# Kernel optimization log

Hardware: AMD Instinct MI355X
Metric: run time of the kernel (lower is better)

The kernel has to match this reference:

```python
import jax, jax.numpy as jnp
import numpy as np

N = 10000   # num_nodes
E = 320000  # num_edges
D = 256     # feature / hidden dim
H = 256


def adj_lap(edge_index, n):
    """Dense normalized adjacency (gcn_norm, no self loops) and sym Laplacian."""
    row, col = edge_index[0], edge_index[1]
    # dense 0/1 adjacency (duplicate edges overwrite with same value, as in the loop)
    A = jnp.zeros((n, n), dtype=jnp.float32).at[row, col].set(1.0)
    # gcn_norm: deg = scatter(w, col) -> column sums
    deg_c = A.sum(axis=0)
    dinv_c = jnp.where(deg_c > 0, jax.lax.rsqrt(jnp.maximum(deg_c, 1e-12)), 0.0)
    anorm = dinv_c[:, None] * A * dinv_c[None, :]
    # get_laplacian 'sym': deg = scatter(w, row) -> row sums; L = I - D^-1/2 A D^-1/2
    deg_r = A.sum(axis=1)
    dinv_r = jnp.where(deg_r > 0, jax.lax.rsqrt(jnp.maximum(deg_r, 1e-12)), 0.0)
    lap = jnp.eye(n, dtype=jnp.float32) - dinv_r[:, None] * A * dinv_r[None, :]
    return lap, anorm


def gcn2(x, M, W1, b1, W2, b2):
    # pretrain_model: two-layer spectral GCN using propagation matrix M
    h = jax.nn.relu(M @ (x @ W1) + b1)
    return M @ (h @ W2) + b2


def setup_inputs() -> dict:
    key = jax.random.key(0)
    k1, k2, k3, k4 = jax.random.split(key, 4)
    x = jax.random.normal(k1, (N, D), dtype=jnp.float32)
    edge_index = jax.random.randint(k2, (2, E), 0, N, dtype=jnp.int64)
    W1 = jax.random.normal(k3, (D, H), dtype=jnp.float32) * 0.05
    b1 = jnp.zeros((H,), dtype=jnp.float32)
    W2 = jax.random.normal(k4, (H, H), dtype=jnp.float32) * 0.05
    b2 = jnp.zeros((H,), dtype=jnp.float32)
    return {"x": x, "edge_index": edge_index, "W1": W1, "b1": b1, "W2": W2, "b2": b2}


def reference(x, edge_index, W1, b1, W2, b2):
    # identity augmentor: x1 = x2 = x, edge_index1 = edge_index2 = edge_index,
    # so adj_lap is identical for both branches (computed once).
    lsym, anorm = adj_lap(edge_index, x.shape[0])
    z1 = gcn2(x, lsym, W1, b1, W2, b2)   # 'high' pass
    z2 = gcn2(x, anorm, W1, b1, W2, b2)  # 'low' pass
    z = z2
    return (z, z1, z2)
```

## Files before the change

kernel.cpp:

```cpp
#include <hip/hip_runtime.h>

#define NN 10000
#define EE 320000
#define HH 256
#define BKT 192

typedef __attribute__((ext_vector_type(8))) short bf16x8;
typedef __attribute__((ext_vector_type(4))) float f32x4;

__device__ float bf2f(unsigned int v) {
    return __uint_as_float(v << 16);
}
__device__ unsigned short f2bf(float f) {
    unsigned int i = __float_as_uint(f);
    return (unsigned short)((i + 0x7fffu + ((i >> 16) & 1u)) >> 16);
}
__device__ unsigned int fp8e(float f) {
    float a = fabsf(f);
    a = fminf(a, 448.0f);
    unsigned int bits = __float_as_uint(a * __uint_as_float(0x03800000u));
    bits = bits + 0x7ffffu + ((bits >> 20) & 1u);
    unsigned int r = bits >> 20;
    if (r > 0x7eu) r = 0x7eu;
    return r | ((__float_as_uint(f) >> 24) & 0x80u);
}
__device__ float fp8d(unsigned int b) {
    float mag = __uint_as_float((b & 0x7fu) << 20) * __uint_as_float(0x7B800000u);
    return __uint_as_float(((b & 0x80u) << 24) | __float_as_uint(mag));
}
__device__ unsigned int pk2(unsigned short a, unsigned short b) {
    return (unsigned int)a | ((unsigned int)b << 16);
}
__device__ int eload(const void* ei, int is64, int idx) {
    if (is64) return (int)(((const long long*)ei)[idx]);
    return ((const int*)ei)[idx];
}
__device__ __forceinline__ float dinv_of(int d) {
    return d > 0 ? rsqrtf((float)d) : 0.0f;
}

__global__ void k_A(const void* x, const void* ei, const void* W1, const void* W2,
                    int* flags, int* rawcnt, unsigned short* W1sw,
                    unsigned short* W2sw) {
    int b = blockIdx.x, t = threadIdx.x;
    if (b >= 65) {
        int idx = (b - 65) * 256 + t;
        ((uint4*)rawcnt)[idx] = make_uint4(0, 0, 0, 0);
        return;
    }
    if (b == 0) {
        __shared__ int s0, s1;
        if (t == 0) { s0 = 0; s1 = 0; }
        __syncthreads();
        if (t < 64) {
            const unsigned int* eu = (const unsigned int*)ei;
            const unsigned int* xu = (const unsigned int*)x;
            for (int k = t; k < 256; k += 64)
                if (eu[2 * k + 1] != 0) atomicOr(&s0, 1);
            unsigned int lo = xu[t] & 0xffffu;
            unsigned int ex = (lo >> 7) & 0xffu;
            if (lo == 0u || (ex >= 90u && ex <= 150u)) atomicAdd(&s1, 1);
        }
        __syncthreads();
        if (t == 0) {
            flags[0] = s0 ? 0 : 1;
            flags[1] = (s1 >= 56) ? 0 : 1;
        }
        return;
    }
    __shared__ int plaus;
    if (t == 0) plaus = 0;
    __syncthreads();
    if (t < 64) {
        unsigned int lo = ((const unsigned int*)x)[t] & 0xffffu;
        unsigned int ex = (lo >> 7) & 0xffu;
        if (lo == 0u || (ex >= 90u && ex <= 150u)) atomicAdd(&plaus, 1);
    }
    __syncthreads();
    int f32io = (plaus >= 56) ? 0 : 1;
    int vb = b - 1;
    const void* W = (vb < 32) ? W1 : W2;
    unsigned short* O = (vb < 32) ? W1sw : W2sw;
    int g = ((vb < 32) ? vb : vb - 32) * 256 + t;
    int gl = g & 63;
    int n = (g >> 6) & 15;
    int ks = g >> 10;
    int coln = n * 16 + (gl & 15);
    int krow = ks * 32 + ((gl >> 4) & 3) * 8;
    unsigned short v[8];
    if (f32io) {
        const float* Wf = (const float*)W;
        #pragma unroll
        for (int j = 0; j < 8; j++) v[j] = f2bf(Wf[(size_t)(krow + j) * HH + coln]);
    } else {
        const unsigned short* Wh = (const unsigned short*)W;
        #pragma unroll
        for (int j = 0; j < 8; j++) v[j] = Wh[(size_t)(krow + j) * HH + coln];
    }
    uint4 p;
    p.x = pk2(v[0], v[1]); p.y = pk2(v[2], v[3]);
    p.z = pk2(v[4], v[5]); p.w = pk2(v[6], v[7]);
    *(uint4*)(O + (size_t)g * 8) = p;
}

__global__ void k_B(const void* x, const void* ei, const unsigned short* W1sw,
                    const int* flags, int* rawcnt, unsigned short* bucket,
                    unsigned char* Yf8, void* Oout) {
    int b = blockIdx.x;
    int tid = threadIdx.x;
    if (b >= 625) {
        int e = (b - 625) * 256 + tid;
        if (e >= EE) return;
        int is64 = flags[0];
        int r = eload(ei, is64, e);
        int c = eload(ei, is64, EE + e);
        if (r < 0 || r >= NN || c < 0 || c >= NN) return;
        int slot = atomicAdd(&rawcnt[r], 1);
        if (slot < BKT) bucket[(size_t)r * BKT + slot] = (unsigned short)c;
        return;
    }
    __shared__ unsigned short As[16][264];
    int r0 = b * 16;
    int af32 = flags[1];
    {
        int row = tid >> 4, seg = tid & 15;
        if (af32) {
            const float* ap = (const float*)x + (size_t)(r0 + row) * HH + seg * 16;
            unsigned short v[16];
            #pragma unroll
            for (int j = 0; j < 16; j += 4) {
                float4 q = *(const float4*)(ap + j);
                v[j] = f2bf(q.x); v[j + 1] = f2bf(q.y);
                v[j + 2] = f2bf(q.z); v[j + 3] = f2bf(q.w);
            }
            uint4 p0, p1;
            p0.x = pk2(v[0], v[1]);   p0.y = pk2(v[2], v[3]);
            p0.z = pk2(v[4], v[5]);   p0.w = pk2(v[6], v[7]);
            p1.x = pk2(v[8], v[9]);   p1.y = pk2(v[10], v[11]);
            p1.z = pk2(v[12], v[13]); p1.w = pk2(v[14], v[15]);
            *(uint4*)&As[row][seg * 16] = p0;
            *(uint4*)&As[row][seg * 16 + 8] = p1;
        } else {
            const unsigned short* ap = (const unsigned short*)x + (size_t)(r0 + row) * HH + seg * 16;
            *(uint4*)&As[row][seg * 16] = *(const uint4*)ap;
            *(uint4*)&As[row][seg * 16 + 8] = *(const uint4*)(ap + 8);
        }
    }
    __syncthreads();
    int wv = tid >> 6;
    int lane = tid & 63;
    int quad = lane >> 4;
    int l16 = lane & 15;
    f32x4 acc[4] = {{0,0,0,0},{0,0,0,0},{0,0,0,0},{0,0,0,0}};
    for (int ks = 0; ks < 8; ks++) {
        bf16x8 af = *(const bf16x8*)&As[l16][ks * 32 + quad * 8];
        #pragma unroll
        for (int t = 0; t < 4; t++) {
            int n = wv * 4 + t;
            bf16x8 bf = *(const bf16x8*)(W1sw + ((size_t)(ks * 16 + n) * 64 + lane) * 8);
            acc[t] = __builtin_amdgcn_mfma_f32_16x16x32_bf16(af, bf, acc[t], 0, 0, 0);
        }
    }
    size_t chunkW = (size_t)NN * HH;
    #pragma unroll
    for (int t = 0; t < 4; t++) {
        int cn = (wv * 4 + t) * 16 + l16;
        #pragma unroll
        for (int r = 0; r < 4; r++) {
            int row = r0 + quad * 4 + r;
            float vv = acc[t][r];
            size_t idx = (size_t)row * HH + cn;
            Yf8[idx] = (unsigned char)fp8e(vv);
            if (af32) ((float*)Oout)[2 * chunkW + idx] = vv;
            else      ((unsigned short*)Oout)[2 * chunkW + idx] = f2bf(vv);
        }
    }
}

__global__ void k_DD(const int* rawcnt, int* cnt2, unsigned short* bucket) {
    __shared__ unsigned int bm[4][316];
    __shared__ int cnt[4];
    int wave = threadIdx.x >> 6;
    int lane = threadIdx.x & 63;
    int i = blockIdx.x * 4 + wave;
    int d = rawcnt[i];
    if (d > BKT) d = BKT;
    for (int t = lane; t < 313; t += 64) bm[wave][t] = 0u;
    if (lane == 0) cnt[wave] = 0;
    unsigned short* bp = bucket + (size_t)i * BKT;
    int cvals[3];
    int nt = 0;
    for (int t = lane; t < d; t += 64) cvals[nt++] = (int)bp[t];
    for (int k = 0; k < nt; k++) {
        int c = cvals[k];
        unsigned int m = 1u << (c & 31);
        unsigned int old = atomicOr(&bm[wave][c >> 5], m);
        if (!(old & m)) {
            int p = atomicAdd(&cnt[wave], 1);
            bp[p] = (unsigned short)c;
            atomicAdd(&cnt2[2 * c + 1], 1);
        }
    }
    if (lane == 0) atomicExch(&cnt2[2 * i], cnt[wave]);
}

__global__ void k_C(const unsigned char* Yf8, const void* Oout,
                    const unsigned short* bucket, const int* cnt2,
                    const void* bias, const int* flags,
                    unsigned short* H1, unsigned short* H2) {
    int wave = threadIdx.x >> 6;
    int lane = threadIdx.x & 63;
    int fb = lane * 4;
    int i = blockIdx.x * 4 + wave;
    float a1[4] = {0, 0, 0, 0};
    float a2[4] = {0, 0, 0, 0};
    int2 ddi = *(const int2*)(cnt2 + 2 * i);
    int n = ddi.x;
    const unsigned short* cp = bucket + (size_t)i * BKT;
    int t = 0;
    for (; t + 4 <= n; t += 4) {
        ushort4 c4 = *(const ushort4*)(cp + t);
        int cx[4] = {(int)c4.x, (int)c4.y, (int)c4.z, (int)c4.w};
        float wx[4], wy[4];
        #pragma unroll
        for (int j = 0; j < 4; j++) {
            int2 dd = *(const int2*)(cnt2 + 2 * cx[j]);
            wx[j] = dinv_of(dd.x);
            wy[j] = dinv_of(dd.y);
        }
        unsigned int gv[4];
        #pragma unroll
        for (int j = 0; j < 4; j++)
            gv[j] = *(const unsigned int*)(Yf8 + (size_t)cx[j] * 256 + fb);
        #pragma unroll
        for (int j = 0; j < 4; j++) {
            #pragma unroll
            for (int k = 0; k < 4; k++) {
                float y = fp8d((gv[j] >> (8 * k)) & 0xffu);
                a1[k] += wx[j] * y;
                a2[k] += wy[j] * y;
            }
        }
    }
    for (; t < n; t++) {
        int c = (int)cp[t];
        int2 dd = *(const int2*)(cnt2 + 2 * c);
        float wx = dinv_of(dd.x);
        float wy = dinv_of(dd.y);
        unsigned int g = *(const unsigned int*)(Yf8 + (size_t)c * 256 + fb);
        #pragma unroll
        for (int k = 0; k < 4; k++) {
            float y = fp8d((g >> (8 * k)) & 0xffu);
            a1[k] += wx * y;
            a2[k] += wy * y;
        }
    }
    int f32io = flags[1];
    float bv[4];
    if (f32io) {
        const float* bp = (const float*)bias + fb;
        #pragma unroll
        for (int k = 0; k < 4; k++) bv[k] = bp[k];
    } else {
        uint2 br = *(const uint2*)((const unsigned short*)bias + fb);
        bv[0] = bf2f(br.x & 0xffffu); bv[1] = bf2f(br.x >> 16);
        bv[2] = bf2f(br.y & 0xffffu); bv[3] = bf2f(br.y >> 16);
    }
    float wiix = dinv_of(ddi.x);
    float wiiy = dinv_of(ddi.y);
    size_t chunkW = (size_t)NN * HH;
    float yv[4];
    if (f32io) {
        const float* sp = (const float*)Oout + 2 * chunkW + (size_t)i * HH + fb;
        #pragma unroll
        for (int k = 0; k < 4; k++) yv[k] = sp[k];
    } else {
        uint2 yi = *(const uint2*)((const unsigned short*)Oout + 2 * chunkW + (size_t)i * HH + fb);
        yv[0] = bf2f(yi.x & 0xffffu); yv[1] = bf2f(yi.x >> 16);
        yv[2] = bf2f(yi.y & 0xffffu); yv[3] = bf2f(yi.y >> 16);
    }
    float h1[4], h2[4];
    #pragma unroll
    for (int k = 0; k < 4; k++) {
        h1[k] = fmaxf(0.f, yv[k] - wiix * a1[k] + bv[k]);
        h2[k] = fmaxf(0.f, wiiy * a2[k] + bv[k]);
    }
    uint2 p1, p2;
    p1.x = pk2(f2bf(h1[0]), f2bf(h1[1])); p1.y = pk2(f2bf(h1[2]), f2bf(h1[3]));
    p2.x = pk2(f2bf(h2[0]), f2bf(h2[1])); p2.y = pk2(f2bf(h2[2]), f2bf(h2[3]));
    *(uint2*)(H1 + (size_t)i * HH + fb) = p1;
    *(uint2*)(H2 + (size_t)i * HH + fb) = p2;
}

__global__ void k_D(const unsigned short* H1, const unsigned short* H2,
                    const unsigned short* Bsw, unsigned char* G12f8,
                    void* Oout, const int* flags) {
    __shared__ unsigned short As[16][264];
    int b = blockIdx.x;
    int tid = threadIdx.x;
    int isG1 = (b < 625);
    const unsigned short* A = isG1 ? H1 : H2;
    int r0 = (isG1 ? b : b - 625) * 16;
    {
        int row = tid >> 4, seg = tid & 15;
        const unsigned short* ap = A + (size_t)(r0 + row) * HH + seg * 16;
        *(uint4*)&As[row][seg * 16] = *(const uint4*)ap;
        *(uint4*)&As[row][seg * 16 + 8] = *(const uint4*)(ap + 8);
    }
    __syncthreads();
    int wv = tid >> 6;
    int lane = tid & 63;
    int quad = lane >> 4;
    int l16 = lane & 15;
    f32x4 acc[4] = {{0,0,0,0},{0,0,0,0},{0,0,0,0},{0,0,0,0}};
    for (int ks = 0; ks < 8; ks++) {
        bf16x8 af = *(const bf16x8*)&As[l16][ks * 32 + quad * 8];
        #pragma unroll
        for (int t = 0; t < 4; t++) {
            int n = wv * 4 + t;
            bf16x8 bf = *(const bf16x8*)(Bsw + ((size_t)(ks * 16 + n) * 64 + lane) * 8);
            acc[t] = __builtin_amdgcn_mfma_f32_16x16x32_bf16(af, bf, acc[t], 0, 0, 0);
        }
    }
    size_t chunkW = (size_t)NN * HH;
    int f32io = flags[1];
    #pragma unroll
    for (int t = 0; t < 4; t++) {
        int cn = (wv * 4 + t) * 16 + l16;
        #pragma unroll
        for (int r = 0; r < 4; r++) {
            int row = r0 + quad * 4 + r;
            float vv = acc[t][r];
            if (isG1) {
                G12f8[(size_t)row * 512 + cn] = (unsigned char)fp8e(vv);
                size_t idx = (size_t)row * HH + cn;
                if (f32io) ((float*)Oout)[chunkW + idx] = vv;
                else       ((unsigned short*)Oout)[chunkW + idx] = f2bf(vv);
            } else {
                G12f8[(size_t)row * 512 + 256 + cn] = (unsigned char)fp8e(vv);
            }
        }
    }
}

__global__ void k_E(const unsigned char* G12f8, const unsigned short* bucket,
                    const int* cnt2, const void* bias, const int* flags,
                    void* Oout) {
    int wave = threadIdx.x >> 6;
    int lane = threadIdx.x & 63;
    int half = lane >> 5;
    int sub = lane & 31;
    int fb = sub * 8;
    int goff = half * 256 + fb;
    int i = blockIdx.x * 4 + wave;
    float acc[8] = {0, 0, 0, 0, 0, 0, 0, 0};
    int2 ddi = *(const int2*)(cnt2 + 2 * i);
    int n = ddi.x;
    const unsigned short* cp = bucket + (size_t)i * BKT;
    int t = 0;
    for (; t + 4 <= n; t += 4) {
        ushort4 c4 = *(const ushort4*)(cp + t);
        int cx[4] = {(int)c4.x, (int)c4.y, (int)c4.z, (int)c4.w};
        float ws[4];
        #pragma unroll
        for (int j = 0; j < 4; j++) {
            int2 dd = *(const int2*)(cnt2 + 2 * cx[j]);
            ws[j] = dinv_of(half ? dd.y : dd.x);
        }
        uint2 gv[4];
        #pragma unroll
        for (int j = 0; j < 4; j++)
            gv[j] = *(const uint2*)(G12f8 + (size_t)cx[j] * 512 + goff);
        #pragma unroll
        for (int j = 0; j < 4; j++) {
            #pragma unroll
            for (int k = 0; k < 4; k++) {
                float y = fp8d((gv[j].x >> (8 * k)) & 0xffu);
                acc[k] += ws[j] * y;
            }
            #pragma unroll
            for (int k = 0; k < 4; k++) {
                float y = fp8d((gv[j].y >> (8 * k)) & 0xffu);
                acc[4 + k] += ws[j] * y;
            }
        }
    }
    for (; t < n; t++) {
        int c = (int)cp[t];
        int2 dd = *(const int2*)(cnt2 + 2 * c);
        float wsel = dinv_of(half ? dd.y : dd.x);
        uint2 g = *(const uint2*)(G12f8 + (size_t)c * 512 + goff);
        #pragma unroll
        for (int k = 0; k < 4; k++) acc[k] += wsel * fp8d((g.x >> (8 * k)) & 0xffu);
        #pragma unroll
        for (int k = 0; k < 4; k++) acc[4 + k] += wsel * fp8d((g.y >> (8 * k)) & 0xffu);
    }
    int f32io = flags[1];
    float bv[8];
    if (f32io) {
        const float* bp = (const float*)bias + fb;
        #pragma unroll
        for (int k = 0; k < 8; k++) bv[k] = bp[k];
    } else {
        uint4 br = *(const uint4*)((const unsigned short*)bias + fb);
        bv[0] = bf2f(br.x & 0xffffu); bv[1] = bf2f(br.x >> 16);
        bv[2] = bf2f(br.y & 0xffffu); bv[3] = bf2f(br.y >> 16);
        bv[4] = bf2f(br.z & 0xffffu); bv[5] = bf2f(br.z >> 16);
        bv[6] = bf2f(br.w & 0xffffu); bv[7] = bf2f(br.w >> 16);
    }
    size_t base = (size_t)i * HH + fb;
    size_t chunkW = (size_t)NN * HH;
    float z[8];
    if (half == 0) {
        float wiix = dinv_of(ddi.x);
        float gvv[8];
        if (f32io) {
            const float* sp = (const float*)Oout + chunkW + base;
            #pragma unroll
            for (int k = 0; k < 8; k++) gvv[k] = sp[k];
        } else {
            uint4 gi = *(const uint4*)((const unsigned short*)Oout + chunkW + base);
            gvv[0] = bf2f(gi.x & 0xffffu); gvv[1] = bf2f(gi.x >> 16);
            gvv[2] = bf2f(gi.y & 0xffffu); gvv[3] = bf2f(gi.y >> 16);
            gvv[4] = bf2f(gi.z & 0xffffu); gvv[5] = bf2f(gi.z >> 16);
            gvv[6] = bf2f(gi.w & 0xffffu); gvv[7] = bf2f(gi.w >> 16);
        }
        #pragma unroll
        for (int k = 0; k < 8; k++) z[k] = gvv[k] - wiix * acc[k] + bv[k];
        if (f32io) {
            float* o = (float*)Oout + chunkW + base;
            *(float4*)o = make_float4(z[0], z[1], z[2], z[3]);
            *(float4*)(o + 4) = make_float4(z[4], z[5], z[6], z[7]);
        } else {
            uint4 p;
            p.x = pk2(f2bf(z[0]), f2bf(z[1])); p.y = pk2(f2bf(z[2]), f2bf(z[3]));
            p.z = pk2(f2bf(z[4]), f2bf(z[5])); p.w = pk2(f2bf(z[6]), f2bf(z[7]));
            *(uint4*)((unsigned short*)Oout + chunkW + base) = p;
        }
    } else {
        float wiiy = dinv_of(ddi.y);
        #pragma unroll
        for (int k = 0; k < 8; k++) z[k] = wiiy * acc[k] + bv[k];
        if (f32io) {
            float* o0 = (float*)Oout + base;
            float* o2 = (float*)Oout + 2 * chunkW + base;
            float4 pa = make_float4(z[0], z[1], z[2], z[3]);
            float4 pb = make_float4(z[4], z[5], z[6], z[7]);
            *(float4*)o0 = pa; *(float4*)(o0 + 4) = pb;
            *(float4*)o2 = pa; *(float4*)(o2 + 4) = pb;
        } else {
            uint4 p;
            p.x = pk2(f2bf(z[0]), f2bf(z[1])); p.y = pk2(f2bf(z[2]), f2bf(z[3]));
            p.z = pk2(f2bf(z[4]), f2bf(z[5])); p.w = pk2(f2bf(z[6]), f2bf(z[7]));
            *(uint4*)((unsigned short*)Oout + base) = p;
            *(uint4*)((unsigned short*)Oout + 2 * chunkW + base) = p;
        }
    }
}

extern "C" void kernel_launch(void* const* d_in, const int* in_sizes, int n_in,
                              void* d_out, int out_size, void* d_ws, size_t ws_size,
                              hipStream_t stream) {
    const void* x = 0; const void* ei = 0;
    const void* W1 = 0; const void* b1 = 0; const void* W2 = 0; const void* b2 = 0;
    for (int i = 0; i < n_in; i++) {
        int s = in_sizes[i];
        if (s == NN * HH) x = d_in[i];
        else if (s == 2 * EE) ei = d_in[i];
        else if (s == HH * HH) { if (!W1) W1 = d_in[i]; else W2 = d_in[i]; }
        else if (s == HH) { if (!b1) b1 = d_in[i]; else b2 = d_in[i]; }
    }

    char* ws = (char*)d_ws;
    size_t off = 0;
    int* flags = (int*)(ws + off); off += 256;
    int* rawcnt = (int*)(ws + off); off += 40960;
    int* cnt2 = (int*)(ws + off); off += 81920;
    unsigned short* bucket = (unsigned short*)(ws + off); off += (size_t)NN * BKT * 2;
    unsigned short* W1sw = (unsigned short*)(ws + off); off += (size_t)HH * HH * 2;
    unsigned short* W2sw = (unsigned short*)(ws + off); off += (size_t)HH * HH * 2;
    unsigned char* Yf8 = (unsigned char*)(ws + off); off += (size_t)NN * 256;
    unsigned char* G12f8 = (unsigned char*)(ws + off); off += (size_t)NN * 512;
    unsigned short* H1 = (unsigned short*)(ws + off); off += (size_t)NN * HH * 2;
    unsigned short* H2 = (unsigned short*)(ws + off); off += (size_t)NN * HH * 2;

    k_A<<<95, 256, 0, stream>>>(x, ei, W1, W2, flags, rawcnt, W1sw, W2sw);
    k_B<<<1875, 256, 0, stream>>>(x, ei, W1sw, flags, rawcnt, bucket, Yf8, d_out);
    k_DD<<<NN / 4, 256, 0, stream>>>(rawcnt, cnt2, bucket);
    k_C<<<NN / 4, 256, 0, stream>>>(Yf8, d_out, bucket, cnt2, b1, flags, H1, H2);
    k_D<<<1250, 256, 0, stream>>>(H1, H2, W2sw, G12f8, d_out, flags);
    k_E<<<NN / 4, 256, 0, stream>>>(G12f8, bucket, cnt2, b2, flags, d_out);
}
```

Measured before the change: 204.4 us.

## Fuse sparse aggregation and W2 GEMM into one kernel via shared-memory H tiles

Merges the first-layer sparse aggregation (k_C) and the second dense GEMM (k_D) into a single kernel. Each 512-thread block aggregates 16 rows, keeps the bf16 H1/H2 tiles in LDS, then runs MFMA against W2 directly. This removes the global H1/H2 round trip and one launch. The cost is only 625 blocks of 512 threads, which lowers parallelism for the gather phase on a large GPU.

```diff
diff --git a/kernel.cpp b/kernel.cpp
--- a/kernel.cpp
+++ b/kernel.cpp
@@ -204,141 +204,128 @@
     if (lane == 0) atomicExch(&cnt2[2 * i], cnt[wave]);
 }
 
-__global__ void k_C(const unsigned char* Yf8, const void* Oout,
-                    const unsigned short* bucket, const int* cnt2,
-                    const void* bias, const int* flags,
-                    unsigned short* H1, unsigned short* H2) {
-    int wave = threadIdx.x >> 6;
-    int lane = threadIdx.x & 63;
+__global__ __launch_bounds__(512) void k_CD(
+        const unsigned char* Yf8, const unsigned short* bucket,
+        const int* cnt2, const unsigned short* W2sw, const void* b1,
+        const int* flags, unsigned char* G12f8, void* Oout) {
+    __shared__ unsigned short H1s[16][264];
+    __shared__ unsigned short H2s[16][264];
+    int tid = threadIdx.x;
+    int wave = tid >> 6;
+    int lane = tid & 63;
     int fb = lane * 4;
-    int i = blockIdx.x * 4 + wave;
-    float a1[4] = {0, 0, 0, 0};
-    float a2[4] = {0, 0, 0, 0};
-    int2 ddi = *(const int2*)(cnt2 + 2 * i);
-    int n = ddi.x;
-    const unsigned short* cp = bucket + (size_t)i * BKT;
-    int t = 0;
-    for (; t + 4 <= n; t += 4) {
-        ushort4 c4 = *(const ushort4*)(cp + t);
-        int cx[4] = {(int)c4.x, (int)c4.y, (int)c4.z, (int)c4.w};
-        float wx[4], wy[4];
-        #pragma unroll
-        for (int j = 0; j < 4; j++) {
-            int2 dd = *(const int2*)(cnt2 + 2 * cx[j]);
-            wx[j] = dinv_of(dd.x);
-            wy[j] = dinv_of(dd.y);
-        }
-        unsigned int gv[4];
-        #pragma unroll
-        for (int j = 0; j < 4; j++)
-            gv[j] = *(const unsigned int*)(Yf8 + (size_t)cx[j] * 256 + fb);
-        #pragma unroll
-        for (int j = 0; j < 4; j++) {
-            #pragma unroll
-            for (int k = 0; k < 4; k++) {
-                float y = fp8d((gv[j] >> (8 * k)) & 0xffu);
-                a1[k] += wx[j] * y;
-                a2[k] += wy[j] * y;
-            }
-        }
-    }
-    for (; t < n; t++) {
-        int c = (int)cp[t];
-        int2 dd = *(const int2*)(cnt2 + 2 * c);
-        float wx = dinv_of(dd.x);
-        float wy = dinv_of(dd.y);
-        unsigned int g = *(const unsigned int*)(Yf8 + (size_t)c * 256 + fb);
-        #pragma unroll
-        for (int k = 0; k < 4; k++) {
-            float y = fp8d((g >> (8 * k)) & 0xffu);
-            a1[k] += wx * y;
-            a2[k] += wy * y;
-        }
-    }
+    int bbase = blockIdx.x * 16;
     int f32io = flags[1];
+    size_t chunkW = (size_t)NN * HH;
     float bv[4];
     if (f32io) {
-        const float* bp = (const float*)bias + fb;
+        const float* bp = (const float*)b1 + fb;
         #pragma unroll
         for (int k = 0; k < 4; k++) bv[k] = bp[k];
     } else {
-        uint2 br = *(const uint2*)((const unsigned short*)bias + fb);
+        uint2 br = *(const uint2*)((const unsigned short*)b1 + fb);
         bv[0] = bf2f(br.x & 0xffffu); bv[1] = bf2f(br.x >> 16);
         bv[2] = bf2f(br.y & 0xffffu); bv[3] = bf2f(br.y >> 16);
     }
-    float wiix = dinv_of(ddi.x);
-    float wiiy = dinv_of(ddi.y);
-    size_t chunkW = (size_t)NN * HH;
-    float yv[4];
-    if (f32io) {
-        const float* sp = (const float*)Oout + 2 * chunkW + (size_t)i * HH + fb;
-        #pragma unroll
-        for (int k = 0; k < 4; k++) yv[k] = sp[k];
-    } else {
-        uint2 yi = *(const uint2*)((const unsigned short*)Oout + 2 * chunkW + (size_t)i * HH + fb);
-        yv[0] = bf2f(yi.x & 0xffffu); yv[1] = bf2f(yi.x >> 16);
-        yv[2] = bf2f(yi.y & 0xffffu); yv[3] = bf2f(yi.y >> 16);
-    }
-    float h1[4], h2[4];
-    #pragma unroll
-    for (int k = 0; k < 4; k++) {
-        h1[k] = fmaxf(0.f, yv[k] - wiix * a1[k] + bv[k]);
-        h2[k] = fmaxf(0.f, wiiy * a2[k] + bv[k]);
-    }
-    uint2 p1, p2;
-    p1.x = pk2(f2bf(h1[0]), f2bf(h1[1])); p1.y = pk2(f2bf(h1[2]), f2bf(h1[3]));
-    p2.x = pk2(f2bf(h2[0]), f2bf(h2[1])); p2.y = pk2(f2bf(h2[2]), f2bf(h2[3]));
-    *(uint2*)(H1 + (size_t)i * HH + fb) = p1;
-    *(uint2*)(H2 + (size_t)i * HH + fb) = p2;
-}
-
-__global__ void k_D(const unsigned short* H1, const unsigned short* H2,
-                    const unsigned short* Bsw, unsigned char* G12f8,
-                    void* Oout, const int* flags) {
-    __shared__ unsigned short As[16][264];
-    int b = blockIdx.x;
-    int tid = threadIdx.x;
-    int isG1 = (b < 625);
-    const unsigned short* A = isG1 ? H1 : H2;
-    int r0 = (isG1 ? b : b - 625) * 16;
-    {
-        int row = tid >> 4, seg = tid & 15;
-        const unsigned short* ap = A + (size_t)(r0 + row) * HH + seg * 16;
-        *(uint4*)&As[row][seg * 16] = *(const uint4*)ap;
-        *(uint4*)&As[row][seg * 16 + 8] = *(const uint4*)(ap + 8);
+    for (int rr = 0; rr < 2; rr++) {
+        int lr = wave * 2 + rr;
+        int i = bbase + lr;
+        float a1[4] = {0, 0, 0, 0};
+        float a2[4] = {0, 0, 0, 0};
+        int2 ddi = *(const int2*)(cnt2 + 2 * i);
+        int n = ddi.x;
+        const unsigned short* cp = bucket + (size_t)i * BKT;
+        int t = 0;
+        for (; t + 4 <= n; t += 4) {
+            ushort4 c4 = *(const ushort4*)(cp + t);
+            int cx[4] = {(int)c4.x, (int)c4.y, (int)c4.z, (int)c4.w};
+            float wx[4], wy[4];
+            #pragma unroll
+            for (int j = 0; j < 4; j++) {
+                int2 dd = *(const int2*)(cnt2 + 2 * cx[j]);
+                wx[j] = dinv_of(dd.x);
+                wy[j] = dinv_of(dd.y);
+            }
+            unsigned int gv[4];
+            #pragma unroll
+            for (int j = 0; j < 4; j++)
+                gv[j] = *(const unsigned int*)(Yf8 + (size_t)cx[j] * 256 + fb);
+            #pragma unroll
+            for (int j = 0; j < 4; j++) {
+                #pragma unroll
+                for (int k = 0; k < 4; k++) {
+                    float y = fp8d((gv[j] >> (8 * k)) & 0xffu);
+                    a1[k] += wx[j] * y;
+                    a2[k] += wy[j] * y;
+                }
+            }
+        }
+        for (; t < n; t++) {
+            int c = (int)cp[t];
+            int2 dd = *(const int2*)(cnt2 + 2 * c);
+            float wx = dinv_of(dd.x);
+            float wy = dinv_of(dd.y);
+            unsigned int g = *(const unsigned int*)(Yf8 + (size_t)c * 256 + fb);
+            #pragma unroll
+            for (int k = 0; k < 4; k++) {
+                float y = fp8d((g >> (8 * k)) & 0xffu);
+                a1[k] += wx * y;
+                a2[k] += wy * y;
+            }
+        }
+        float wiix = dinv_of(ddi.x);
+        float wiiy = dinv_of(ddi.y);
+        float yv[4];
+        if (f32io) {
+            const float* sp = (const float*)Oout + 2 * chunkW + (size_t)i * HH + fb;
+            #pragma unroll
+            for (int k = 0; k < 4; k++) yv[k] = sp[k];
+        } else {
+            uint2 yi = *(const uint2*)((const unsigned short*)Oout + 2 * chunkW + (size_t)i * HH + fb);
+            yv[0] = bf2f(yi.x & 0xffffu); yv[1] = bf2f(yi.x >> 16);
+            yv[2] = bf2f(yi.y & 0xffffu); yv[3] = bf2f(yi.y >> 16);
+        }
+        float h1[4], h2[4];
+        #pragma unroll
+        for (int k = 0; k < 4; k++) {
+            h1[k] = fmaxf(0.f, yv[k] - wiix * a1[k] + bv[k]);
+            h2[k] = fmaxf(0.f, wiiy * a2[k] + bv[k]);
+        }
+        uint2 p1, p2;
+        p1.x = pk2(f2bf(h1[0]), f2bf(h1[1])); p1.y = pk2(f2bf(h1[2]), f2bf(h1[3]));
+        p2.x = pk2(f2bf(h2[0]), f2bf(h2[1])); p2.y = pk2(f2bf(h2[2]), f2bf(h2[3]));
+        *(uint2*)&H1s[lr][fb] = p1;
+        *(uint2*)&H2s[lr][fb] = p2;
     }
     __syncthreads();
-    int wv = tid >> 6;
-    int lane = tid & 63;
     int quad = lane >> 4;
     int l16 = lane & 15;
-    f32x4 acc[4] = {{0,0,0,0},{0,0,0,0},{0,0,0,0},{0,0,0,0}};
+    f32x4 acc1[2] = {{0,0,0,0},{0,0,0,0}};
+    f32x4 acc2[2] = {{0,0,0,0},{0,0,0,0}};
     for (int ks = 0; ks < 8; ks++) {
-        bf16x8 af = *(const bf16x8*)&As[l16][ks * 32 + quad * 8];
-        #pragma unroll
-        for (int t = 0; t < 4; t++) {
-            int n = wv * 4 + t;
-            bf16x8 bf = *(const bf16x8*)(Bsw + ((size_t)(ks * 16 + n) * 64 + lane) * 8);
-            acc[t] = __builtin_amdgcn_mfma_f32_16x16x32_bf16(af, bf, acc[t], 0, 0, 0);
-        }
-    }
-    size_t chunkW = (size_t)NN * HH;
-    int f32io = flags[1];
+        bf16x8 af1 = *(const bf16x8*)&H1s[l16][ks * 32 + quad * 8];
+        bf16x8 af2 = *(const bf16x8*)&H2s[l16][ks * 32 + quad * 8];
+        #pragma unroll
+        for (int t = 0; t < 2; t++) {
+            int n = wave * 2 + t;
+            bf16x8 bf = *(const bf16x8*)(W2sw + ((size_t)(ks * 16 + n) * 64 + lane) * 8);
+            acc1[t] = __builtin_amdgcn_mfma_f32_16x16x32_bf16(af1, bf, acc1[t], 0, 0, 0);
+            acc2[t] = __builtin_amdgcn_mfma_f32_16x16x32_bf16(af2, bf, acc2[t], 0, 0, 0);
+        }
+    }
     #pragma unroll
-    for (int t = 0; t < 4; t++) {
-        int cn = (wv * 4 + t) * 16 + l16;
+    for (int t = 0; t < 2; t++) {
+        int cn = (wave * 2 + t) * 16 + l16;
         #pragma unroll
         for (int r = 0; r < 4; r++) {
-            int row = r0 + quad * 4 + r;
-            float vv = acc[t][r];
-            if (isG1) {
-                G12f8[(size_t)row * 512 + cn] = (unsigned char)fp8e(vv);
-                size_t idx = (size_t)row * HH + cn;
-                if (f32io) ((float*)Oout)[chunkW + idx] = vv;
-                else       ((unsigned short*)Oout)[chunkW + idx] = f2bf(vv);
-            } else {
-                G12f8[(size_t)row * 512 + 256 + cn] = (unsigned char)fp8e(vv);
-            }
+            int row = bbase + quad * 4 + r;
+            float v1 = acc1[t][r];
+            float v2 = acc2[t][r];
+            G12f8[(size_t)row * 512 + cn] = (unsigned char)fp8e(v1);
+            G12f8[(size_t)row * 512 + 256 + cn] = (unsigned char)fp8e(v2);
+            size_t idx = (size_t)row * HH + cn;
+            if (f32io) ((float*)Oout)[chunkW + idx] = v1;
+            else       ((unsigned short*)Oout)[chunkW + idx] = f2bf(v1);
         }
     }
 }
@@ -481,13 +468,10 @@
     unsigned short* W2sw = (unsigned short*)(ws + off); off += (size_t)HH * HH * 2;
     unsigned char* Yf8 = (unsigned char*)(ws + off); off += (size_t)NN * 256;
     unsigned char* G12f8 = (unsigned char*)(ws + off); off += (size_t)NN * 512;
-    unsigned short* H1 = (unsigned short*)(ws + off); off += (size_t)NN * HH * 2;
-    unsigned short* H2 = (unsigned short*)(ws + off); off += (size_t)NN * HH * 2;
 
     k_A<<<95, 256, 0, stream>>>(x, ei, W1, W2, flags, rawcnt, W1sw, W2sw);
     k_B<<<1875, 256, 0, stream>>>(x, ei, W1sw, flags, rawcnt, bucket, Yf8, d_out);
     k_DD<<<NN / 4, 256, 0, stream>>>(rawcnt, cnt2, bucket);
-    k_C<<<NN / 4, 256, 0, stream>>>(Yf8, d_out, bucket, cnt2, b1, flags, H1, H2);
-    k_D<<<1250, 256, 0, stream>>>(H1, H2, W2sw, G12f8, d_out, flags);
+    k_CD<<<625, 512, 0, stream>>>(Yf8, bucket, cnt2, W2sw, b1, flags, G12f8, d_out);
     k_E<<<NN / 4, 256, 0, stream>>>(G12f8, bucket, cnt2, b2, flags, d_out);
 }
```

After: 204.3 us. About the same (-0.1%).
